# Kernel tuning notes

Measured on AMD Instinct MI355X. Metric: run time of the kernel, lower is better.

## Reference

```python
import jax, jax.numpy as jnp
import numpy as np

DIM = 512
HEADS = 8
DIM_HEAD = 64
INNER = HEADS * DIM_HEAD  # 512
SCALE = DIM_HEAD ** -0.5


def setup_inputs() -> dict:
    key = jax.random.key(0)
    k1, k2, k3, k4 = jax.random.split(key, 4)
    x = jax.random.normal(k1, (4, 2048, DIM), dtype=jnp.float32)
    # Dense(inner_dim*3, use_bias=False): weight [dim, 3*inner]
    w_qkv = jax.random.normal(k2, (DIM, 3 * INNER), dtype=jnp.float32) * (DIM ** -0.5)
    # to_out Dense(dim): weight [inner, dim] + bias [dim]
    w_out = jax.random.normal(k3, (INNER, DIM), dtype=jnp.float32) * (INNER ** -0.5)
    b_out = jax.random.normal(k4, (DIM,), dtype=jnp.float32) * 0.01
    return {"x": x, "w_qkv": w_qkv, "w_out": w_out, "b_out": b_out}


def reference(x, w_qkv, w_out, b_out):
    b, n, _ = x.shape
    qkv = x @ w_qkv                                  # [b, n, 3*inner]
    q, k, v = jnp.split(qkv, 3, axis=-1)             # each [b, n, inner]
    def to_heads(t):
        return t.reshape(b, n, HEADS, DIM_HEAD).transpose(0, 2, 1, 3)  # [b, h, n, d]
    q, k, v = map(to_heads, (q, k, v))
    dots = jnp.einsum('bhid,bhjd->bhij', q, k) * SCALE
    attn = jax.nn.softmax(dots, axis=-1)
    out = jnp.einsum('bhij,bhjd->bhid', attn, v)     # [b, h, n, d]
    out = out.transpose(0, 2, 1, 3).reshape(b, n, INNER)
    return out @ w_out + b_out                       # [b, n, dim]
```

## Files before the change

kernel.cpp:

```cpp
#include <hip/hip_runtime.h>
#include <stdint.h>

#define DIM    512
#define HEADS  8
#define DHEAD  64
#define SEQ    2048
#define BATCH  4
#define BH     (BATCH*HEADS)
#define MROWS  (BATCH*SEQ)
#define NQKV   (3*DIM)
#define QSCALE 0.18033688011112042f

typedef __bf16 bf16x8 __attribute__((ext_vector_type(8)));
typedef float  f32x4  __attribute__((ext_vector_type(4)));
typedef float  f32x16 __attribute__((ext_vector_type(16)));

typedef unsigned short u16;

#if __has_builtin(__builtin_amdgcn_exp2f)
#define EXP2(x) __builtin_amdgcn_exp2f(x)
#else
#define EXP2(x) exp2f(x)
#endif

__device__ __forceinline__ u16 f2bf(float f) {
    union { float f; uint32_t u; } v; v.f = f;
    uint32_t u = v.u;
    uint32_t r = (u + 0x7FFFu + ((u >> 16) & 1u)) >> 16;
    return (u16)r;
}
__device__ __forceinline__ float bf2f(u16 h) {
    union { uint32_t u; float f; } v; v.u = ((uint32_t)h) << 16;
    return v.f;
}
__device__ __forceinline__ uint32_t pk2bf(float a, float b) {
    union { float f; uint32_t u; } ua, ub; ua.f = a; ub.f = b;
#if __has_builtin(__builtin_amdgcn_perm)
    return __builtin_amdgcn_perm(ub.u + 0x8000u, ua.u + 0x8000u, 0x07060302u);
#else
    return ((ua.u + 0x8000u) >> 16) | ((ub.u + 0x8000u) & 0xFFFF0000u);
#endif
}

#define P32SWAP(x, y) asm("v_permlane32_swap_b32 %0, %1" : "+v"(x), "+v"(y))

__device__ __forceinline__ void async16(const void* g, u16* l) {
    __builtin_amdgcn_global_load_lds(
        (const __attribute__((address_space(1))) void*)g,
        (__attribute__((address_space(3))) void*)l, 16, 0, 0);
}

#define XBLKS (MROWS * DIM / 4 / 256)
#define WQT   ((DIM / 64) * (NQKV / 64))
#define WOT   ((DIM / 64) * (DIM / 64))
__global__ void prep(const void* __restrict__ x, const void* __restrict__ wq,
                     const void* __restrict__ wo, u16* __restrict__ xb,
                     u16* __restrict__ wtq, u16* __restrict__ wto,
                     int* __restrict__ flag) {
    __shared__ int cnt;
    __shared__ __align__(16) u16 tile[64][72];
    int tid = threadIdx.x;
    if (tid == 0) cnt = 0;
    __syncthreads();
    {
        u16 v = ((const u16*)x)[tid * 2];
        int e = (v >> 7) & 0xFF;
        atomicAdd(&cnt, (v == 0) || (e >= 100 && e <= 140));
    }
    __syncthreads();
    int isbf = (cnt >= 192);
    int b = blockIdx.x;
    if (b == 0 && tid == 0) *flag = isbf;

    if (b < XBLKS) {
        int i = b * 256 + tid;
        if (isbf) {
            ((uint2*)xb)[i] = ((const uint2*)x)[i];
        } else {
            float4 v = ((const float4*)x)[i];
            ushort4 o;
            o.x = f2bf(v.x); o.y = f2bf(v.y); o.z = f2bf(v.z); o.w = f2bf(v.w);
            ((ushort4*)xb)[i] = o;
        }
        return;
    }
    const void* W; u16* Wt; int N, tb;
    if (b < XBLKS + WQT) { W = wq; Wt = wtq; N = NQKV; tb = b - XBLKS; }
    else                 { W = wo; Wt = wto; N = DIM;  tb = b - XBLKS - WQT; }
    int tn = N / 64;
    int k0 = (tb / tn) * 64, n0 = (tb - (tb / tn) * tn) * 64;

#pragma unroll 4
    for (int it = 0; it < 16; ++it) {
        int idx = it * 256 + tid;
        int r = idx >> 6, c = idx & 63;
        u16 v = isbf ? ((const u16*)W)[(size_t)(k0 + r) * N + n0 + c]
                     : f2bf(((const float*)W)[(size_t)(k0 + r) * N + n0 + c]);
        tile[c][r] = v;
    }
    __syncthreads();
    {
        int n = tid >> 2, ks = (tid & 3) * 16;
        uint4 v0 = *(const uint4*)&tile[n][ks];
        uint4 v1 = *(const uint4*)&tile[n][ks + 8];
        *(uint4*)&Wt[(size_t)(n0 + n) * DIM + k0 + ks] = v0;
        *(uint4*)&Wt[(size_t)(n0 + n) * DIM + k0 + ks + 8] = v1;
    }
}

template<int KDIM, int TM, int TN>
__device__ __forceinline__ void gemm_lds_db(
        const u16* __restrict__ A, const u16* __restrict__ Bt,
        int m0, int n0, int tid, u16* As, u16* Bs,
        f32x4 (&acc)[TM / 32][TN / 32]) {
    int lane = tid & 63, ln = lane & 15, quad = lane >> 4, w = tid >> 6;
    int wm = (w >> 1) * (TM / 2), wn = (w & 1) * (TN / 2);

    auto stage = [&](int buf, int k0) {
#pragma unroll
        for (int ii = 0; ii < TM / 64; ++ii) {
            int r0 = (ii * 4 + w) * 16;
            int row = r0 + (lane >> 2);
            int seg = (lane & 3) ^ (row & 3);
            async16(A + (size_t)(m0 + row) * KDIM + k0 + seg * 8,
                    As + buf * TM * 32 + r0 * 32);
        }
#pragma unroll
        for (int ii = 0; ii < TN / 64; ++ii) {
            int r0 = (ii * 4 + w) * 16;
            int row = r0 + (lane >> 2);
            int seg = (lane & 3) ^ (row & 3);
            async16(Bt + (size_t)(n0 + row) * KDIM + k0 + seg * 8,
                    Bs + buf * TN * 32 + r0 * 32);
        }
    };

    stage(0, 0);
#pragma unroll 1
    for (int kk = 0; kk < KDIM / 32; ++kk) {
        __syncthreads();
        if (kk + 1 < KDIM / 32) stage((kk + 1) & 1, (kk + 1) * 32);
        const u16* Ac = As + (kk & 1) * TM * 32;
        const u16* Bc = Bs + (kk & 1) * TN * 32;
        bf16x8 a[TM / 32], b[TN / 32];
        int rseg = (quad ^ (ln & 3)) * 8;
#pragma unroll
        for (int i = 0; i < TM / 32; ++i)
            a[i] = *(const bf16x8*)(Ac + (wm + i * 16 + ln) * 32 + rseg);
#pragma unroll
        for (int j = 0; j < TN / 32; ++j)
            b[j] = *(const bf16x8*)(Bc + (wn + j * 16 + ln) * 32 + rseg);
#pragma unroll
        for (int i = 0; i < TM / 32; ++i)
#pragma unroll
            for (int j = 0; j < TN / 32; ++j)
                acc[i][j] = __builtin_amdgcn_mfma_f32_16x16x32_bf16(
                    a[i], b[j], acc[i][j], 0, 0, 0);
    }
}

__global__ __launch_bounds__(256, 3) void qkv_gemm(
        const u16* __restrict__ X, const u16* __restrict__ Wt,
        u16* __restrict__ Qt, u16* __restrict__ Kb, u16* __restrict__ Vt) {
    __shared__ __align__(16) u16 As[2 * 128 * 32];
    __shared__ __align__(16) u16 Bs[2 * 128 * 32];

    int tid  = threadIdx.x;
    int lane = tid & 63, ln = lane & 15, quad = lane >> 4, wid = tid >> 6;
    int m0 = blockIdx.x * 128, n0 = blockIdx.y * 128;
    int wm = (wid >> 1) * 64, wn = (wid & 1) * 64;

    f32x4 acc[4][4];
#pragma unroll
    for (int i = 0; i < 4; ++i)
#pragma unroll
        for (int j = 0; j < 4; ++j) acc[i][j] = 0.f;

    gemm_lds_db<DIM, 128, 128>(X, Wt, m0, n0, tid, As, Bs, acc);

#pragma unroll
    for (int j = 0; j < 4; ++j) {
        int col   = n0 + wn + j * 16 + ln;
        int which = col >> 9;
        int hd    = col & 511;
        int h     = hd >> 6, d = hd & 63;
#pragma unroll
        for (int i = 0; i < 4; ++i) {
            int rbase = m0 + wm + i * 16 + quad * 4;
            int b = rbase >> 11, n = rbase & 2047;
            int bh = b * HEADS + h;
            if (which == 1) {
#pragma unroll
                for (int r = 0; r < 4; ++r)
                    Kb[((size_t)bh * SEQ + n + r) * DHEAD + d] = f2bf(acc[i][j][r]);
            } else {
                float s = (which == 0) ? QSCALE : 1.0f;
                uint2 pv;
                pv.x = pk2bf(acc[i][j][0] * s, acc[i][j][1] * s);
                pv.y = pk2bf(acc[i][j][2] * s, acc[i][j][3] * s);
                u16* dst = (which == 0) ? Qt : Vt;
                *(uint2*)&dst[((size_t)bh * DHEAD + d) * SEQ + n] = pv;
            }
        }
    }
}

__global__ __launch_bounds__(256, 2) void flash_attn(
        const u16* __restrict__ Qt, const u16* __restrict__ Kb,
        const u16* __restrict__ Vt, u16* __restrict__ Ob) {
    __shared__ __align__(16) u16 Kc[2][64 * 64];
    __shared__ __align__(16) u16 Vc[2][64 * 64];

    int tid  = threadIdx.x;
    int lane = tid & 63, c = lane & 31, hi = lane >> 5, wid = tid >> 6;
    int bh = blockIdx.x;
    int q0 = blockIdx.y * 128 + wid * 32;

    const u16* Qh = Qt + (size_t)bh * SEQ * DHEAD;
    const u16* Kh = Kb + (size_t)bh * SEQ * DHEAD;
    const u16* Vh = Vt + (size_t)bh * DHEAD * SEQ;

    int srow = lane >> 3;
    auto stageKV = [&](int buf, int kc) {
#pragma unroll
        for (int ii = 0; ii < 2; ++ii) {
            int slab = wid + ii * 4;
            int g = (lane & 7) ^ srow ^ (slab & 3);
            const u16* gk = Kh + (size_t)(kc + slab * 8 + srow) * DHEAD + g * 8;
            async16(gk, &Kc[buf][slab * 8 * 64]);
            const u16* gv = Vh + (size_t)(slab * 8 + srow) * SEQ + kc + g * 8;
            async16(gv, &Vc[buf][slab * 8 * 64]);
        }
    };

    bf16x8 qf[4];
#pragma unroll
    for (int ds = 0; ds < 4; ++ds) {
        union { u16 a[8]; bf16x8 v; } u;
#pragma unroll
        for (int j = 0; j < 8; ++j)
            u.a[j] = Qh[(size_t)(ds * 16 + hi * 8 + j) * SEQ + q0 + c];
        qf[ds] = u.v;
    }

    bf16x8 onesf;
    { union { uint32_t d[4]; bf16x8 v; } u;
      u.d[0] = u.d[1] = u.d[2] = u.d[3] = 0x3F803F80u; onesf = u.v; }

    f32x16 o[2];
    f32x16 lacc;
    lacc = 0.f;
#pragma unroll
    for (int dt = 0; dt < 2; ++dt) o[dt] = 0.f;

    stageKV(0, 0);
    __syncthreads();

    int fl = (c & 7) ^ ((c >> 3) & 3);

#pragma unroll 1
    for (int kc = 0; kc < SEQ; kc += 64) {
        int cur = (kc >> 6) & 1;
        if (kc + 64 < SEQ) stageKV(cur ^ 1, kc + 64);

#pragma unroll
        for (int kt = 0; kt < 2; ++kt) {
            bf16x8 kf[4];
#pragma unroll
            for (int ds = 0; ds < 4; ++ds) {
                int slot = (ds * 2 + hi) ^ fl;
                kf[ds] = *(const bf16x8*)&Kc[cur][(kt * 32 + c) * 64 + slot * 8];
            }

            f32x16 s;
            s = 0.f;
            __builtin_amdgcn_s_setprio(1);
#pragma unroll
            for (int ds = 0; ds < 4; ++ds)
                s = __builtin_amdgcn_mfma_f32_32x32x16_bf16(
                    kf[ds], qf[ds], s, 0, 0, 0);
            __builtin_amdgcn_s_setprio(0);

            float p[16];
#pragma unroll
            for (int r = 0; r < 16; ++r) p[r] = EXP2(s[r]);
            uint32_t X[8];
#pragma unroll
            for (int i = 0; i < 8; ++i) X[i] = pk2bf(p[2 * i], p[2 * i + 1]);
            P32SWAP(X[0], X[2]); P32SWAP(X[1], X[3]);
            P32SWAP(X[4], X[6]); P32SWAP(X[5], X[7]);
            bf16x8 pa[2];
            union { uint32_t d[4]; bf16x8 v; } u0, u1;
            u0.d[0] = X[0]; u0.d[1] = X[1]; u0.d[2] = X[2]; u0.d[3] = X[3];
            u1.d[0] = X[4]; u1.d[1] = X[5]; u1.d[2] = X[6]; u1.d[3] = X[7];
            pa[0] = u0.v; pa[1] = u1.v;

            __builtin_amdgcn_s_setprio(1);
#pragma unroll
            for (int tl = 0; tl < 2; ++tl) {
#pragma unroll
                for (int dt = 0; dt < 2; ++dt) {
                    int slot = ((kt * 2 + tl) * 2 + hi) ^ fl;
                    bf16x8 vf = *(const bf16x8*)&Vc[cur][(dt * 32 + c) * 64 + slot * 8];
                    o[dt] = __builtin_amdgcn_mfma_f32_32x32x16_bf16(
                        pa[tl], vf, o[dt], 0, 0, 0);
                }
                lacc = __builtin_amdgcn_mfma_f32_32x32x16_bf16(
                    pa[tl], onesf, lacc, 0, 0, 0);
            }
            __builtin_amdgcn_s_setprio(0);
        }
        __syncthreads();
    }

    int b = bh >> 3, hh = bh & 7;
    f32x16 linv;
#pragma unroll
    for (int r = 0; r < 16; ++r) linv[r] = 1.0f / lacc[r];
#pragma unroll
    for (int dt = 0; dt < 2; ++dt)
#pragma unroll
        for (int r = 0; r < 16; ++r) {
            int ql = (r & 3) + 8 * (r >> 2) + 4 * hi;
            int n  = q0 + ql;
            int d  = dt * 32 + c;
            Ob[((size_t)(b * SEQ + n)) * DIM + hh * DHEAD + d] =
                f2bf(o[dt][r] * linv[r]);
        }
}

__global__ __launch_bounds__(256, 3) void out_gemm(
        const u16* __restrict__ A, const u16* __restrict__ Wt,
        const void* __restrict__ bias, void* __restrict__ out,
        const int* __restrict__ flag) {
    __shared__ __align__(16) u16 As[2 * 64 * 32];
    __shared__ __align__(16) u16 Bs[2 * 128 * 32];

    int tid  = threadIdx.x;
    int lane = tid & 63, ln = lane & 15, quad = lane >> 4, wid = tid >> 6;
    int m0 = blockIdx.x * 64, n0 = blockIdx.y * 128;
    int wm = (wid >> 1) * 32, wn = (wid & 1) * 64;
    int isbf = *flag;

    f32x4 acc[2][4];
#pragma unroll
    for (int i = 0; i < 2; ++i)
#pragma unroll
        for (int j = 0; j < 4; ++j) acc[i][j] = 0.f;

    gemm_lds_db<DIM, 64, 128>(A, Wt, m0, n0, tid, As, Bs, acc);

#pragma unroll
    for (int j = 0; j < 4; ++j) {
        int col = n0 + wn + j * 16 + ln;
        float bv = isbf ? bf2f(((const u16*)bias)[col])
                        : ((const float*)bias)[col];
#pragma unroll
        for (int i = 0; i < 2; ++i) {
            int rbase = m0 + wm + i * 16 + quad * 4;
#pragma unroll
            for (int r = 0; r < 4; ++r) {
                int row = rbase + r;
                size_t off = (size_t)row * DIM + col;
                float val = acc[i][j][r] + bv;
                if (isbf) ((u16*)out)[off] = f2bf(val);
                else      ((float*)out)[off] = val;
            }
        }
    }
}

extern "C" void kernel_launch(void* const* d_in, const int* in_sizes, int n_in,
                              void* d_out, int out_size, void* d_ws, size_t ws_size,
                              hipStream_t stream) {
    const void* x     = d_in[0];
    const void* w_qkv = d_in[1];
    const void* w_out = d_in[2];
    const void* b_out = d_in[3];

    int* flag   = (int*)d_ws;
    u16* x_bf   = (u16*)((char*)d_ws + 16);
    u16* wt_qkv = x_bf + (size_t)MROWS * DIM;
    u16* wt_out = wt_qkv + (size_t)NQKV * DIM;
    u16* Qt     = wt_out + (size_t)DIM * DIM;
    u16* Kb     = Qt + (size_t)BH * SEQ * DHEAD;
    u16* Vt     = Kb + (size_t)BH * SEQ * DHEAD;
    u16* attn   = x_bf;

    prep<<<XBLKS + WQT + WOT, 256, 0, stream>>>(
        x, w_qkv, w_out, x_bf, wt_qkv, wt_out, flag);
    qkv_gemm<<<dim3(MROWS / 128, NQKV / 128), 256, 0, stream>>>(x_bf, wt_qkv, Qt, Kb, Vt);
    flash_attn<<<dim3(BH, SEQ / 128), 256, 0, stream>>>(Qt, Kb, Vt, attn);
    out_gemm<<<dim3(MROWS / 64, DIM / 128), 256, 0, stream>>>(attn, wt_out, b_out, d_out, flag);
}
```

Before: 174.4 us.

## Split attention key chunks across two waves per query tile and combine via LDS

The flash attention block grows from 256 to 512 threads. Each pair of waves shares a 32-row query tile, and each wave handles half of every 64-key chunk, so each K/V tile is staged once for twice as many waves. The row-sum is now computed with scalar adds plus a cross-half shuffle, replacing the extra ones-vector MFMA. Partial outputs and sums are combined through LDS after the loop. This is meant to raise wave-level parallelism and latency hiding, at the cost of an LDS reduction epilogue, extra barriers, and higher register and LDS pressure under the launch_bounds(512,4) target.

```diff
diff --git a/kernel.cpp b/kernel.cpp
--- a/kernel.cpp
+++ b/kernel.cpp
@@ -205,16 +205,21 @@
     }
 }
 
-__global__ __launch_bounds__(256, 2) void flash_attn(
+__global__ __launch_bounds__(512, 4) void flash_attn(
         const u16* __restrict__ Qt, const u16* __restrict__ Kb,
         const u16* __restrict__ Vt, u16* __restrict__ Ob) {
-    __shared__ __align__(16) u16 Kc[2][64 * 64];
-    __shared__ __align__(16) u16 Vc[2][64 * 64];
+    __shared__ __align__(16) u16 SMEM[18432];
+    __shared__ float Lcomb[4][32];
+    __shared__ float Lq[4][32];
+    u16* Kc0 = SMEM;
+    u16* Vc0 = SMEM + 8192;
+    float* OC = (float*)SMEM;
 
     int tid  = threadIdx.x;
     int lane = tid & 63, c = lane & 31, hi = lane >> 5, wid = tid >> 6;
+    int ws = wid & 1, wq = wid >> 1;
     int bh = blockIdx.x;
-    int q0 = blockIdx.y * 128 + wid * 32;
+    int q0 = blockIdx.y * 128 + wq * 32;
 
     const u16* Qh = Qt + (size_t)bh * SEQ * DHEAD;
     const u16* Kh = Kb + (size_t)bh * SEQ * DHEAD;
@@ -222,15 +227,12 @@
 
     int srow = lane >> 3;
     auto stageKV = [&](int buf, int kc) {
-#pragma unroll
-        for (int ii = 0; ii < 2; ++ii) {
-            int slab = wid + ii * 4;
-            int g = (lane & 7) ^ srow ^ (slab & 3);
-            const u16* gk = Kh + (size_t)(kc + slab * 8 + srow) * DHEAD + g * 8;
-            async16(gk, &Kc[buf][slab * 8 * 64]);
-            const u16* gv = Vh + (size_t)(slab * 8 + srow) * SEQ + kc + g * 8;
-            async16(gv, &Vc[buf][slab * 8 * 64]);
-        }
+        int slab = wid;
+        int g = (lane & 7) ^ srow ^ (slab & 3);
+        const u16* gk = Kh + (size_t)(kc + slab * 8 + srow) * DHEAD + g * 8;
+        async16(gk, Kc0 + buf * 4096 + slab * 8 * 64);
+        const u16* gv = Vh + (size_t)(slab * 8 + srow) * SEQ + kc + g * 8;
+        async16(gv, Vc0 + buf * 4096 + slab * 8 * 64);
     };
 
     bf16x8 qf[4];
@@ -243,13 +245,8 @@
         qf[ds] = u.v;
     }
 
-    bf16x8 onesf;
-    { union { uint32_t d[4]; bf16x8 v; } u;
-      u.d[0] = u.d[1] = u.d[2] = u.d[3] = 0x3F803F80u; onesf = u.v; }
-
     f32x16 o[2];
-    f32x16 lacc;
-    lacc = 0.f;
+    float lsum = 0.f;
 #pragma unroll
     for (int dt = 0; dt < 2; ++dt) o[dt] = 0.f;
 
@@ -263,70 +260,111 @@
         int cur = (kc >> 6) & 1;
         if (kc + 64 < SEQ) stageKV(cur ^ 1, kc + 64);
 
-#pragma unroll
-        for (int kt = 0; kt < 2; ++kt) {
-            bf16x8 kf[4];
-#pragma unroll
-            for (int ds = 0; ds < 4; ++ds) {
-                int slot = (ds * 2 + hi) ^ fl;
-                kf[ds] = *(const bf16x8*)&Kc[cur][(kt * 32 + c) * 64 + slot * 8];
-            }
-
-            f32x16 s;
-            s = 0.f;
-            __builtin_amdgcn_s_setprio(1);
-#pragma unroll
-            for (int ds = 0; ds < 4; ++ds)
-                s = __builtin_amdgcn_mfma_f32_32x32x16_bf16(
-                    kf[ds], qf[ds], s, 0, 0, 0);
-            __builtin_amdgcn_s_setprio(0);
-
-            float p[16];
-#pragma unroll
-            for (int r = 0; r < 16; ++r) p[r] = EXP2(s[r]);
-            uint32_t X[8];
-#pragma unroll
-            for (int i = 0; i < 8; ++i) X[i] = pk2bf(p[2 * i], p[2 * i + 1]);
-            P32SWAP(X[0], X[2]); P32SWAP(X[1], X[3]);
-            P32SWAP(X[4], X[6]); P32SWAP(X[5], X[7]);
-            bf16x8 pa[2];
-            union { uint32_t d[4]; bf16x8 v; } u0, u1;
-            u0.d[0] = X[0]; u0.d[1] = X[1]; u0.d[2] = X[2]; u0.d[3] = X[3];
-            u1.d[0] = X[4]; u1.d[1] = X[5]; u1.d[2] = X[6]; u1.d[3] = X[7];
-            pa[0] = u0.v; pa[1] = u1.v;
-
-            __builtin_amdgcn_s_setprio(1);
-#pragma unroll
-            for (int tl = 0; tl < 2; ++tl) {
-#pragma unroll
-                for (int dt = 0; dt < 2; ++dt) {
-                    int slot = ((kt * 2 + tl) * 2 + hi) ^ fl;
-                    bf16x8 vf = *(const bf16x8*)&Vc[cur][(dt * 32 + c) * 64 + slot * 8];
-                    o[dt] = __builtin_amdgcn_mfma_f32_32x32x16_bf16(
-                        pa[tl], vf, o[dt], 0, 0, 0);
-                }
-                lacc = __builtin_amdgcn_mfma_f32_32x32x16_bf16(
-                    pa[tl], onesf, lacc, 0, 0, 0);
-            }
-            __builtin_amdgcn_s_setprio(0);
-        }
+        const u16* Kcur = Kc0 + cur * 4096;
+        const u16* Vcur = Vc0 + cur * 4096;
+
+        bf16x8 kf[4];
+#pragma unroll
+        for (int ds = 0; ds < 4; ++ds) {
+            int slot = (ds * 2 + hi) ^ fl;
+            kf[ds] = *(const bf16x8*)&Kcur[(ws * 32 + c) * 64 + slot * 8];
+        }
+
+        f32x16 s;
+        s = 0.f;
+        __builtin_amdgcn_s_setprio(1);
+#pragma unroll
+        for (int ds = 0; ds < 4; ++ds)
+            s = __builtin_amdgcn_mfma_f32_32x32x16_bf16(
+                kf[ds], qf[ds], s, 0, 0, 0);
+        __builtin_amdgcn_s_setprio(0);
+
+        float p[16];
+#pragma unroll
+        for (int r = 0; r < 16; ++r) p[r] = EXP2(s[r]);
+        {
+            float t0 = (p[0] + p[1]) + (p[2] + p[3]);
+            float t1 = (p[4] + p[5]) + (p[6] + p[7]);
+            float t2 = (p[8] + p[9]) + (p[10] + p[11]);
+            float t3 = (p[12] + p[13]) + (p[14] + p[15]);
+            lsum += (t0 + t1) + (t2 + t3);
+        }
+        uint32_t X[8];
+#pragma unroll
+        for (int i = 0; i < 8; ++i) X[i] = pk2bf(p[2 * i], p[2 * i + 1]);
+        P32SWAP(X[0], X[2]); P32SWAP(X[1], X[3]);
+        P32SWAP(X[4], X[6]); P32SWAP(X[5], X[7]);
+        bf16x8 pa[2];
+        union { uint32_t d[4]; bf16x8 v; } u0, u1;
+        u0.d[0] = X[0]; u0.d[1] = X[1]; u0.d[2] = X[2]; u0.d[3] = X[3];
+        u1.d[0] = X[4]; u1.d[1] = X[5]; u1.d[2] = X[6]; u1.d[3] = X[7];
+        pa[0] = u0.v; pa[1] = u1.v;
+
+        __builtin_amdgcn_s_setprio(1);
+#pragma unroll
+        for (int tl = 0; tl < 2; ++tl)
+#pragma unroll
+            for (int dt = 0; dt < 2; ++dt) {
+                int slot = ((ws * 2 + tl) * 2 + hi) ^ fl;
+                bf16x8 vf = *(const bf16x8*)&Vcur[(dt * 32 + c) * 64 + slot * 8];
+                o[dt] = __builtin_amdgcn_mfma_f32_32x32x16_bf16(
+                    pa[tl], vf, o[dt], 0, 0, 0);
+            }
+        __builtin_amdgcn_s_setprio(0);
+
         __syncthreads();
     }
 
-    int b = bh >> 3, hh = bh & 7;
-    f32x16 linv;
-#pragma unroll
-    for (int r = 0; r < 16; ++r) linv[r] = 1.0f / lacc[r];
-#pragma unroll
-    for (int dt = 0; dt < 2; ++dt)
-#pragma unroll
-        for (int r = 0; r < 16; ++r) {
-            int ql = (r & 3) + 8 * (r >> 2) + 4 * hi;
-            int n  = q0 + ql;
-            int d  = dt * 32 + c;
-            Ob[((size_t)(b * SEQ + n)) * DIM + hh * DHEAD + d] =
-                f2bf(o[dt][r] * linv[r]);
-        }
+    lsum += __shfl_xor(lsum, 32);
+
+    if (ws == 1) {
+#pragma unroll
+        for (int dt = 0; dt < 2; ++dt) {
+            int base = (((wq * 2 + dt) * 2 + hi) * 32 + c) * 18;
+#pragma unroll
+            for (int g = 0; g < 4; ++g) {
+                f32x4 v;
+                v[0] = o[dt][g * 4 + 0]; v[1] = o[dt][g * 4 + 1];
+                v[2] = o[dt][g * 4 + 2]; v[3] = o[dt][g * 4 + 3];
+                *(f32x4*)&OC[base + g * 4] = v;
+            }
+        }
+        if (hi == 0) Lcomb[wq][c] = lsum;
+    }
+    __syncthreads();
+    if (ws == 0) {
+#pragma unroll
+        for (int dt = 0; dt < 2; ++dt) {
+            int base = (((wq * 2 + dt) * 2 + hi) * 32 + c) * 18;
+#pragma unroll
+            for (int g = 0; g < 4; ++g) {
+                f32x4 v = *(const f32x4*)&OC[base + g * 4];
+                o[dt][g * 4 + 0] += v[0]; o[dt][g * 4 + 1] += v[1];
+                o[dt][g * 4 + 2] += v[2]; o[dt][g * 4 + 3] += v[3];
+            }
+        }
+        float ltot = lsum + Lcomb[wq][c];
+        if (hi == 0) Lq[wq][c] = ltot;
+    }
+    __syncthreads();
+
+    if (ws == 0) {
+        int b = bh >> 3, hh = bh & 7;
+        f32x16 linv;
+#pragma unroll
+        for (int r = 0; r < 16; ++r)
+            linv[r] = 1.0f / Lq[wq][(r & 3) + 8 * (r >> 2) + 4 * hi];
+#pragma unroll
+        for (int dt = 0; dt < 2; ++dt)
+#pragma unroll
+            for (int r = 0; r < 16; ++r) {
+                int ql = (r & 3) + 8 * (r >> 2) + 4 * hi;
+                int n  = q0 + ql;
+                int d  = dt * 32 + c;
+                Ob[((size_t)(b * SEQ + n)) * DIM + hh * DHEAD + d] =
+                    f2bf(o[dt][r] * linv[r]);
+            }
+    }
 }
 
 __global__ __launch_bounds__(256, 3) void out_gemm(
@@ -390,6 +428,6 @@
     prep<<<XBLKS + WQT + WOT, 256, 0, stream>>>(
         x, w_qkv, w_out, x_bf, wt_qkv, wt_out, flag);
     qkv_gemm<<<dim3(MROWS / 128, NQKV / 128), 256, 0, stream>>>(x_bf, wt_qkv, Qt, Kb, Vt);
-    flash_attn<<<dim3(BH, SEQ / 128), 256, 0, stream>>>(Qt, Kb, Vt, attn);
+    flash_attn<<<dim3(BH, SEQ / 128), 512, 0, stream>>>(Qt, Kb, Vt, attn);
     out_gemm<<<dim3(MROWS / 64, DIM / 128), 256, 0, stream>>>(attn, wt_out, b_out, d_out, flag);
 }
```

Measured after the change: 176.3 us. Within noise of the previous version (+1.1%).
